# Performance work log

Hardware: AMD Instinct MI355X
Metric: run time of the kernel (lower is better)

## Reference

```python
import jax, jax.numpy as jnp
import numpy as np

DIM = 128
N_CENTERS = 30
CUT_LO, CUT_HI = 0.0, 10.0
N_CONV = 3
NODE_VOCAB = 100
EDGE_VOCAB = 500
N_NODES = 50000
N_EDGES = 800000
N_GRAPHS = 100
DIM_E = DIM + N_CENTERS  # 158


def setup_inputs() -> dict:
    key = jax.random.key(0)
    ks = jax.random.split(key, 20)
    def xav(k, shape):
        fan_in = shape[-2] if len(shape) >= 2 else shape[-1]
        return (jax.random.normal(k, shape, dtype=jnp.float32) / np.sqrt(fan_in)).astype(jnp.float32)
    inp = {
        'node_types': jax.random.randint(ks[0], (N_NODES,), 0, NODE_VOCAB),
        'edge_types': jax.random.randint(ks[1], (N_EDGES,), 0, EDGE_VOCAB),
        'src': jax.random.randint(ks[2], (N_EDGES,), 0, N_NODES),
        'dst': jax.random.randint(ks[3], (N_EDGES,), 0, N_NODES),
        'graph_ids': jnp.sort(jax.random.randint(ks[4], (N_NODES,), 0, N_GRAPHS)),
        'distances': jax.random.uniform(ks[5], (N_EDGES,), dtype=jnp.float32, minval=CUT_LO, maxval=CUT_HI),
        'n_graphs': N_GRAPHS,
        # embedding tables
        'node_emb': xav(ks[6], (NODE_VOCAB, DIM)),
        'edge_emb': xav(ks[7], (EDGE_VOCAB, DIM)),
        # stacked per-conv-layer weights (n_conv leading dim)
        'Wn1': xav(ks[8], (N_CONV, DIM, DIM)),  'bn1': jnp.zeros((N_CONV, DIM), jnp.float32),
        'Wn2': xav(ks[9], (N_CONV, DIM, DIM)),  'bn2': jnp.zeros((N_CONV, DIM), jnp.float32),
        'We1': xav(ks[10], (N_CONV, DIM_E, DIM)), 'be1': jnp.zeros((N_CONV, DIM), jnp.float32),
        'We2': xav(ks[11], (N_CONV, DIM, DIM)),  'be2': jnp.zeros((N_CONV, DIM), jnp.float32),
        'Wc':  xav(ks[12], (N_CONV, DIM, DIM)),  'bc': jnp.zeros((N_CONV, DIM), jnp.float32),
        # read layer
        'Wr1': xav(ks[13], (DIM, DIM)), 'br1': jnp.zeros((DIM,), jnp.float32),
        'Wr2': xav(ks[14], (DIM, 1)),   'br2': jnp.zeros((1,), jnp.float32),
    }
    return inp


def reference(node_types, edge_types, src, dst, graph_ids, distances, n_graphs,
              node_emb, edge_emb, Wn1, bn1, Wn2, bn2, We1, be1, We2, be2, Wc, bc,
              Wr1, br1, Wr2, br2):
    # embeddings
    h = node_emb[node_types]                      # [N, D]
    e_emb = edge_emb[edge_types]                  # [E, D]
    # RBF expansion of distances
    centers = jnp.linspace(CUT_LO, CUT_HI, N_CENTERS, dtype=jnp.float32)
    gap = centers[1] - centers[0]
    rbf = jnp.exp(-((distances[:, None] - centers[None, :]) ** 2) / gap)  # [E, n_centers]
    e = jnp.concatenate([e_emb, rbf], axis=1)     # [E, D + n_centers]

    n_nodes = h.shape[0]
    for i in range(N_CONV):
        node_path = jnp.maximum(h[src] @ Wn1[i] + bn1[i], 0.0) @ Wn2[i] + bn2[i]   # [E, D]
        edge_path = jnp.maximum(e @ We1[i] + be1[i], 0.0) @ We2[i] + be2[i]        # [E, D]
        m = jnp.tanh((node_path * edge_path) @ Wc[i] + bc[i])                       # [E, D]
        h = h + jax.ops.segment_sum(m, dst, num_segments=n_nodes)                   # scatter-add to dst

    # readout MLP + per-graph node sum
    hr = jnp.maximum(h @ Wr1 + br1, 0.0) @ Wr2 + br2                                # [N, 1]
    out = jax.ops.segment_sum(hr, graph_ids, num_segments=n_graphs)                 # [G, 1]
    return out.reshape(-1)
```

## Files before the change

kernel.cpp:

```cpp
#include <hip/hip_runtime.h>
#include <stdint.h>

#define NNODES 50000
#define NEDGES 800000
#define NGRAPH 100
#define NCHUNK (NEDGES / 16)
#define NWAVES 4096
#define NB0 196

typedef _Float16 f16;
typedef __attribute__((ext_vector_type(8))) _Float16 half8;
typedef __attribute__((ext_vector_type(4))) _Float16 half4;
typedef __attribute__((ext_vector_type(4))) float floatx4;

__device__ __forceinline__ void stage_WT(const float* __restrict__ W, f16* WT,
                                         int tid, int nthr) {
    for (int idx = tid; idx < 128 * 32; idx += nthr) {
        int k = idx >> 5, n4 = (idx & 31) * 4;
        floatx4 v = *(const floatx4*)(W + k * 128 + n4);
        WT[(n4 + 0) * 136 + k] = (f16)v[0];
        WT[(n4 + 1) * 136 + k] = (f16)v[1];
        WT[(n4 + 2) * 136 + k] = (f16)v[2];
        WT[(n4 + 3) * 136 + k] = (f16)v[3];
    }
}

__device__ __forceinline__ float fast_tanh(float x) {
    x = fminf(fmaxf(x, -15.0f), 15.0f);
    float e2 = __expf(2.0f * x);
    return (e2 - 1.0f) * __builtin_amdgcn_rcpf(e2 + 1.0f);
}

__device__ __forceinline__ int mtAddr(int c, int rgroup) {
    return c * 16 + ((((c >> 2) + rgroup) & 3) << 2);
}

__global__ void init_k(float* out, int osz, int* cnt) {
    int i = blockIdx.x * 256 + threadIdx.x;
    if (i < osz) out[i] = 0.0f;
    if (i < NNODES) cnt[i] = 0;
}

__global__ void hist_k(const int* __restrict__ dst, int* __restrict__ cnt) {
    int e = blockIdx.x * 256 + threadIdx.x;
    if (e < NEDGES) atomicAdd(&cnt[dst[e]], 1);
}

__global__ __launch_bounds__(1024) void scan1_k(const int* __restrict__ cnt,
                                                int* __restrict__ rowStart,
                                                int* __restrict__ blockSum) {
    __shared__ int buf[1024];
    int tid = threadIdx.x;
    int i = blockIdx.x * 1024 + tid;
    int v = (i < NNODES) ? cnt[i] : 0;
    buf[tid] = v;
    __syncthreads();
    for (int off = 1; off < 1024; off <<= 1) {
        int t = (tid >= off) ? buf[tid - off] : 0;
        __syncthreads();
        buf[tid] += t;
        __syncthreads();
    }
    if (i < NNODES) rowStart[i] = buf[tid] - v;
    if (tid == 1023) blockSum[blockIdx.x] = buf[1023];
}

__global__ void scan2_k(int* __restrict__ blockSum, int nb) {
    if (threadIdx.x == 0) {
        int run = 0;
        for (int b = 0; b < nb; ++b) { int s = blockSum[b]; blockSum[b] = run; run += s; }
    }
}

__global__ __launch_bounds__(1024) void scan3_k(int* __restrict__ rowStart,
                                                const int* __restrict__ blockSum,
                                                int* __restrict__ cnt) {
    int i = blockIdx.x * 1024 + threadIdx.x;
    if (i < NNODES) { rowStart[i] += blockSum[blockIdx.x]; cnt[i] = 0; }
    if (i == 0) rowStart[NNODES] = NEDGES;
}

__global__ void scatter_k(const int* __restrict__ src, const int* __restrict__ et,
                          const int* __restrict__ dst, const float* __restrict__ dist,
                          const int* __restrict__ rowStart, int* __restrict__ cnt,
                          uint4* __restrict__ packE) {
    int e = blockIdx.x * 256 + threadIdx.x;
    if (e >= NEDGES) return;
    int d = dst[e];
    int pos = rowStart[d] + atomicAdd(&cnt[d], 1);
    uint4 pk;
    pk.x = (unsigned)src[e];
    pk.y = (unsigned)et[e];
    pk.z = (unsigned)d;
    pk.w = __float_as_uint(dist[e]);
    packE[pos] = pk;
}

__global__ void gather_h(const int* __restrict__ nt, const float* __restrict__ emb,
                         float* __restrict__ h) {
    int i = blockIdx.x * 256 + threadIdx.x;
    int row = i >> 5, c4 = (i & 31) * 4;
    if (row < NNODES)
        *(floatx4*)(h + row * 128 + c4) = *(const floatx4*)(emb + nt[row] * 128 + c4);
}

__global__ __launch_bounds__(1024, 4) void mlp_combo(
        const float* __restrict__ Xh,
        const float* __restrict__ W1, const float* __restrict__ b1,
        const float* __restrict__ W2, const float* __restrict__ b2,
        f16* __restrict__ OutP,
        const float* __restrict__ Xe,
        const float* __restrict__ We1, const float* __restrict__ be1,
        f16* __restrict__ OutT) {
    __shared__ f16 W1T[128 * 136];
    __shared__ f16 W2T[128 * 136];
    __shared__ f16 xBuf[256 * 136];
    __shared__ float bias1[128];
    __shared__ float bias2[128];
    int tid = threadIdx.x;
    bool mode2 = blockIdx.x >= NB0;

    const float* X  = mode2 ? Xe : Xh;
    const float* Wa = mode2 ? We1 : W1;
    const float* ba = mode2 ? be1 : b1;
    f16* Out        = mode2 ? OutT : OutP;
    int  M          = mode2 ? 500 : NNODES;
    int  r0         = (mode2 ? (blockIdx.x - NB0) : blockIdx.x) * 256;

    stage_WT(Wa, W1T, tid, 1024);
    if (!mode2) stage_WT(W2, W2T, tid, 1024);
    if (tid < 128) { bias1[tid] = ba[tid]; bias2[tid] = mode2 ? 0.0f : b2[tid]; }

    for (int it = 0; it < 8; ++it) {
        int row = it * 32 + (tid >> 5);
        int c4 = (tid & 31) * 4;
        int gr = r0 + row;
        floatx4 x = {0.0f, 0.0f, 0.0f, 0.0f};
        if (gr < M) x = *(const floatx4*)(X + (size_t)gr * 128 + c4);
        half4 xh;
        xh[0] = (f16)x[0]; xh[1] = (f16)x[1]; xh[2] = (f16)x[2]; xh[3] = (f16)x[3];
        *(half4*)(xBuf + row * 136 + c4) = xh;
    }
    __syncthreads();

    int lane = tid & 63, wv = tid >> 6;
    int R = wv * 16;
    int n16 = lane & 15, q = lane >> 4;
    int gr = r0 + R + n16;

    half8 a[4];
    #pragma unroll
    for (int kk = 0; kk < 4; ++kk)
        a[kk] = *(const half8*)(xBuf + (R + n16) * 136 + kk * 32 + q * 8);

    #pragma unroll
    for (int f = 0; f < 8; ++f) {
        floatx4 acc = *(const floatx4*)(bias1 + f * 16 + q * 4);
        #pragma unroll
        for (int kk = 0; kk < 4; ++kk) {
            half8 aw = *(const half8*)(W1T + (f * 16 + n16) * 136 + kk * 32 + q * 8);
            acc = __builtin_amdgcn_mfma_f32_16x16x32_f16(aw, a[kk], acc, 0, 0, 0);
        }
        if (!mode2) {
            half4 y;
            #pragma unroll
            for (int i = 0; i < 4; ++i) y[i] = (f16)fmaxf(acc[i], 0.0f);
            *(half4*)(xBuf + (R + n16) * 136 + f * 16 + q * 4) = y;
        } else {
            half4 o;
            #pragma unroll
            for (int i = 0; i < 4; ++i) o[i] = (f16)acc[i];
            if (gr < M) *(half4*)(Out + (size_t)gr * 128 + f * 16 + q * 4) = o;
        }
    }

    if (!mode2) {
        #pragma unroll
        for (int kk = 0; kk < 4; ++kk)
            a[kk] = *(const half8*)(xBuf + (R + n16) * 136 + kk * 32 + q * 8);
        #pragma unroll
        for (int f = 0; f < 8; ++f) {
            floatx4 acc = *(const floatx4*)(bias2 + f * 16 + q * 4);
            #pragma unroll
            for (int kk = 0; kk < 4; ++kk) {
                half8 aw = *(const half8*)(W2T + (f * 16 + n16) * 136 + kk * 32 + q * 8);
                acc = __builtin_amdgcn_mfma_f32_16x16x32_f16(aw, a[kk], acc, 0, 0, 0);
            }
            half4 o;
            #pragma unroll
            for (int i = 0; i < 4; ++i) o[i] = (f16)acc[i];
            if (gr < M) *(half4*)(Out + (size_t)gr * 128 + f * 16 + q * 4) = o;
        }
    }
}

__global__ __launch_bounds__(1024, 4) void edge_kernel(
        const uint4* __restrict__ packE,
        const f16* __restrict__ P, const f16* __restrict__ T,
        const float* __restrict__ We1,
        const float* __restrict__ We2, const float* __restrict__ be2,
        const float* __restrict__ Wc,  const float* __restrict__ bc,
        float* __restrict__ h) {
    __shared__ f16 W2T[128 * 136];
    __shared__ f16 WcT[128 * 136];
    __shared__ f16 W1rT[128 * 40];
    __shared__ f16 Uall[16 * 2176];
    __shared__ float sbe2[128], sbc[128];
    __shared__ int dstW[16][16];

    int tid = threadIdx.x;
    stage_WT(We2, W2T, tid, 1024);
    stage_WT(Wc,  WcT, tid, 1024);
    for (int idx = tid; idx < 128 * 32; idx += 1024) {
        int n = idx >> 5, kr = idx & 31;
        W1rT[n * 40 + kr] = (kr < 30) ? (f16)We1[(128 + kr) * 128 + n] : (f16)0.0f;
    }
    if (tid < 128) { sbe2[tid] = be2[tid]; sbc[tid] = bc[tid]; }
    __syncthreads();

    int lane = tid & 63, wv = tid >> 6;
    f16* U = Uall + wv * 2176;
    int* dW = dstW[wv];
    int n16 = lane & 15, q = lane >> 4;
    const float invgap = 29.0f / 10.0f;
    int colA = lane, colB = lane + 64;
    int tsub = lane & 3, trow = lane >> 2;

    float sbcv[8];
    #pragma unroll
    for (int f = 0; f < 8; ++f) sbcv[f] = sbc[f * 16 + n16];

    int wgid = blockIdx.x * 16 + wv;
    int extra = wgid < 848 ? wgid : 848;
    int c0 = wgid * 12 + extra;
    int c1 = c0 + 12 + (wgid < 848 ? 1 : 0);

    float carry0 = 0.0f, carry1 = 0.0f;
    int prev = -1;

    uint4 pk = {0u, 0u, 0u, 0u};
    if (lane < 16) pk = packE[(size_t)c0 * 16 + lane];

    for (int ch = c0; ch < c1; ++ch) {
        bool hasNext = (ch + 1 < c1);
        int   ety  = __shfl((int)pk.y, trow);
        int   srcv = __shfl((int)pk.x, n16);
        float dcur = __shfl(__uint_as_float(pk.w), n16);
        if (lane < 16) dW[lane] = (int)pk.z;

        {
            const uint4* Tp = (const uint4*)(T + (size_t)ety * 128 + tsub * 32);
            uint4 tr0 = Tp[0], tr1 = Tp[1], tr2 = Tp[2], tr3 = Tp[3];
            uint4* ub = (uint4*)(U + trow * 136 + tsub * 32);
            ub[0] = tr0; ub[1] = tr1; ub[2] = tr2; ub[3] = tr3;
        }
        __builtin_amdgcn_sched_barrier(0);

        half8 pA0, pA1, pA2, pA3;
        {
            const f16* Pr = P + (size_t)srcv * 128 + q * 8;
            pA0 = *(const half8*)(Pr);
            pA1 = *(const half8*)(Pr + 32);
            pA2 = *(const half8*)(Pr + 64);
            pA3 = *(const half8*)(Pr + 96);
        }
        uint4 pkn = {0u, 0u, 0u, 0u};
        if (hasNext && lane < 16) pkn = packE[(size_t)(ch + 1) * 16 + lane];

        half8 ar;
        #pragma unroll
        for (int j = 0; j < 8; ++j) {
            int k = q * 8 + j;
            float c = (float)k * (10.0f / 29.0f);
            float df = dcur - c;
            ar[j] = (f16)((k < 30) ? __expf(-df * df * invgap) : 0.0f);
        }

        #pragma unroll
        for (int f = 0; f < 8; ++f) {
            f16* up = U + n16 * 136 + f * 16 + q * 4;
            half4 tv = *(const half4*)up;
            floatx4 c4 = {(float)tv[0], (float)tv[1], (float)tv[2], (float)tv[3]};
            half8 aw = *(const half8*)(W1rT + (f * 16 + n16) * 40 + q * 8);
            c4 = __builtin_amdgcn_mfma_f32_16x16x32_f16(aw, ar, c4, 0, 0, 0);
            half4 uv;
            #pragma unroll
            for (int i = 0; i < 4; ++i) uv[i] = (f16)fmaxf(c4[i], 0.0f);
            *(half4*)up = uv;
        }

        half8 a2[4];
        #pragma unroll
        for (int kk = 0; kk < 4; ++kk)
            a2[kk] = *(const half8*)(U + n16 * 136 + kk * 32 + q * 8);
        #pragma unroll
        for (int f = 0; f < 8; ++f) {
            floatx4 acc = *(const floatx4*)(sbe2 + f * 16 + q * 4);
            #pragma unroll
            for (int kk = 0; kk < 4; ++kk) {
                half8 aw = *(const half8*)(W2T + (f * 16 + n16) * 136 + kk * 32 + q * 8);
                acc = __builtin_amdgcn_mfma_f32_16x16x32_f16(aw, a2[kk], acc, 0, 0, 0);
            }
            half4 ev;
            #pragma unroll
            for (int i = 0; i < 4; ++i) ev[i] = (f16)acc[i];
            *(half4*)(U + n16 * 136 + f * 16 + q * 4) = ev;
        }

        {
            half8 e0 = *(const half8*)(U + n16 * 136 + 0 * 32 + q * 8);
            half8 e1 = *(const half8*)(U + n16 * 136 + 1 * 32 + q * 8);
            half8 e2 = *(const half8*)(U + n16 * 136 + 2 * 32 + q * 8);
            half8 e3 = *(const half8*)(U + n16 * 136 + 3 * 32 + q * 8);
            a2[0] = e0 * pA0; a2[1] = e1 * pA1; a2[2] = e2 * pA2; a2[3] = e3 * pA3;
        }
        #pragma unroll
        for (int f = 0; f < 8; ++f) {
            float bb = sbcv[f];
            floatx4 acc = {bb, bb, bb, bb};
            #pragma unroll
            for (int kk = 0; kk < 4; ++kk) {
                half8 b = *(const half8*)(WcT + (f * 16 + n16) * 136 + kk * 32 + q * 8);
                acc = __builtin_amdgcn_mfma_f32_16x16x32_f16(a2[kk], b, acc, 0, 0, 0);
            }
            int c = f * 16 + n16;
            half4 mv;
            #pragma unroll
            for (int i = 0; i < 4; ++i) mv[i] = (f16)fast_tanh(acc[i]);
            *(half4*)(U + mtAddr(c, q)) = mv;
        }

        {
            half4 va[4], vb[4];
            #pragma unroll
            for (int g2 = 0; g2 < 4; ++g2) {
                va[g2] = *(const half4*)(U + mtAddr(colA, g2));
                vb[g2] = *(const half4*)(U + mtAddr(colB, g2));
            }
            int dArr[16];
            *(int4*)(dArr)      = *(const int4*)(dW);
            *(int4*)(dArr + 4)  = *(const int4*)(dW + 4);
            *(int4*)(dArr + 8)  = *(const int4*)(dW + 8);
            *(int4*)(dArr + 12) = *(const int4*)(dW + 12);
            #pragma unroll
            for (int r = 0; r < 16; ++r) {
                int dd = dArr[r];
                float v0 = (float)va[r >> 2][r & 3];
                float v1 = (float)vb[r >> 2][r & 3];
                if (dd != prev) {
                    if (prev >= 0) {
                        unsafeAtomicAdd(&h[(size_t)prev * 128 + colA], carry0);
                        unsafeAtomicAdd(&h[(size_t)prev * 128 + colB], carry1);
                    }
                    prev = dd; carry0 = v0; carry1 = v1;
                } else { carry0 += v0; carry1 += v1; }
            }
        }
        pk = pkn;
        __builtin_amdgcn_sched_barrier(0);
    }
    if (prev >= 0) {
        unsafeAtomicAdd(&h[(size_t)prev * 128 + colA], carry0);
        unsafeAtomicAdd(&h[(size_t)prev * 128 + colB], carry1);
    }
}

__global__ __launch_bounds__(1024, 4) void readout_k(
        const float* __restrict__ X, int M,
        const float* __restrict__ W1, const float* __restrict__ b1,
        const float* __restrict__ Wr2, const float* __restrict__ br2,
        const int* __restrict__ gid, float* __restrict__ out) {
    __shared__ f16 W1T[128 * 136];
    __shared__ f16 xBuf[256 * 136];
    __shared__ float bias1[128];
    __shared__ float sWr2[128];
    int tid = threadIdx.x;

    stage_WT(W1, W1T, tid, 1024);
    if (tid < 128) { bias1[tid] = b1[tid]; sWr2[tid] = Wr2[tid]; }

    int r0 = blockIdx.x * 256;
    for (int it = 0; it < 8; ++it) {
        int row = it * 32 + (tid >> 5);
        int c4 = (tid & 31) * 4;
        int gr = r0 + row;
        floatx4 x = {0.0f, 0.0f, 0.0f, 0.0f};
        if (gr < M) x = *(const floatx4*)(X + (size_t)gr * 128 + c4);
        half4 xh;
        xh[0] = (f16)x[0]; xh[1] = (f16)x[1]; xh[2] = (f16)x[2]; xh[3] = (f16)x[3];
        *(half4*)(xBuf + row * 136 + c4) = xh;
    }
    __syncthreads();

    int lane = tid & 63, wv = tid >> 6;
    int R = wv * 16;
    int n16 = lane & 15, q = lane >> 4;

    half8 a[4];
    #pragma unroll
    for (int kk = 0; kk < 4; ++kk)
        a[kk] = *(const half8*)(xBuf + (R + n16) * 136 + kk * 32 + q * 8);

    floatx4 acc[8];
    #pragma unroll
    for (int f = 0; f < 8; ++f) {
        float bb = bias1[f * 16 + n16];
        acc[f] = (floatx4){bb, bb, bb, bb};
        #pragma unroll
        for (int kk = 0; kk < 4; ++kk) {
            half8 b = *(const half8*)(W1T + (f * 16 + n16) * 136 + kk * 32 + q * 8);
            acc[f] = __builtin_amdgcn_mfma_f32_16x16x32_f16(a[kk], b, acc[f], 0, 0, 0);
        }
    }

    float s[4];
    #pragma unroll
    for (int i = 0; i < 4; ++i) {
        float t = 0.0f;
        #pragma unroll
        for (int f = 0; f < 8; ++f)
            t += fmaxf(acc[f][i], 0.0f) * sWr2[f * 16 + n16];
        #pragma unroll
        for (int m = 1; m < 16; m <<= 1) t += __shfl_xor(t, m);
        s[i] = t;
    }

    if (n16 == 0) {
        float br2v = br2[0];
        float t = 0.0f; int g = -1;
        #pragma unroll
        for (int i = 0; i < 4; ++i) {
            int gr = r0 + R + q * 4 + i;
            if (gr < M) {
                int gi = gid[gr];
                float si = s[i] + br2v;
                if (gi == g) t += si;
                else { if (g >= 0) unsafeAtomicAdd(&out[g], t); g = gi; t = si; }
            }
        }
        if (g >= 0) unsafeAtomicAdd(&out[g], t);
    }
}

extern "C" void kernel_launch(void* const* d_in, const int* in_sizes, int n_in,
                              void* d_out, int out_size, void* d_ws, size_t ws_size,
                              hipStream_t stream) {
    (void)in_sizes; (void)n_in; (void)ws_size;
    const int*   node_types = (const int*)d_in[0];
    const int*   edge_types = (const int*)d_in[1];
    const int*   src        = (const int*)d_in[2];
    const int*   dst        = (const int*)d_in[3];
    const int*   graph_ids  = (const int*)d_in[4];
    const float* distances  = (const float*)d_in[5];
    const float* node_emb   = (const float*)d_in[7];
    const float* edge_emb   = (const float*)d_in[8];
    const float* Wn1 = (const float*)d_in[9];
    const float* bn1 = (const float*)d_in[10];
    const float* Wn2 = (const float*)d_in[11];
    const float* bn2 = (const float*)d_in[12];
    const float* We1 = (const float*)d_in[13];
    const float* be1 = (const float*)d_in[14];
    const float* We2 = (const float*)d_in[15];
    const float* be2 = (const float*)d_in[16];
    const float* Wc  = (const float*)d_in[17];
    const float* bc  = (const float*)d_in[18];
    const float* Wr1 = (const float*)d_in[19];
    const float* br1 = (const float*)d_in[20];
    const float* Wr2 = (const float*)d_in[21];
    const float* br2 = (const float*)d_in[22];

    char* w = (char*)d_ws;
    auto carve = [&](size_t bytes) { char* p = w; w += (bytes + 255) & ~(size_t)255; return p; };
    float* h        = (float*)carve((size_t)NNODES * 128 * 4);
    f16*   P        = (f16*)  carve((size_t)NNODES * 128 * 2);
    f16*   T        = (f16*)  carve((size_t)500 * 128 * 2);
    int*   rowStart = (int*)  carve((size_t)(NNODES + 1) * 4);
    int*   cnt      = (int*)  carve((size_t)NNODES * 4);
    int*   blockSum = (int*)  carve((size_t)64 * 4);
    uint4* packE    = (uint4*)carve((size_t)NEDGES * 16);

    float* out = (float*)d_out;
    const int NB1 = (NNODES + 1023) / 1024;

    init_k<<<(NNODES + 255) / 256, 256, 0, stream>>>(out, out_size, cnt);
    hist_k<<<NEDGES / 256, 256, 0, stream>>>(dst, cnt);
    scan1_k<<<NB1, 1024, 0, stream>>>(cnt, rowStart, blockSum);
    scan2_k<<<1, 64, 0, stream>>>(blockSum, NB1);
    scan3_k<<<NB1, 1024, 0, stream>>>(rowStart, blockSum, cnt);
    scatter_k<<<NEDGES / 256, 256, 0, stream>>>(src, edge_types, dst, distances,
                                                rowStart, cnt, packE);
    gather_h<<<(NNODES * 32 + 255) / 256, 256, 0, stream>>>(node_types, node_emb, h);

    for (int i = 0; i < 3; ++i) {
        mlp_combo<<<NB0 + 2, 1024, 0, stream>>>(
            h, Wn1 + (size_t)i * 128 * 128, bn1 + i * 128,
            Wn2 + (size_t)i * 128 * 128, bn2 + i * 128, P,
            edge_emb, We1 + (size_t)i * 158 * 128, be1 + i * 128, T);
        edge_kernel<<<256, 1024, 0, stream>>>(
            packE, P, T,
            We1 + (size_t)i * 158 * 128,
            We2 + (size_t)i * 128 * 128, be2 + i * 128,
            Wc + (size_t)i * 128 * 128, bc + i * 128, h);
    }

    readout_k<<<(NNODES + 255) / 256, 1024, 0, stream>>>(
        h, NNODES, Wr1, br1, Wr2, br2, graph_ids, out);
}
```

Before: 678.8 us.

## Fuse CSR preprocessing kernels into one cooperative kernel with grid syncs

Replaces seven small preprocessing launches (init, histogram, three-stage scan, scatter, embedding gather) with a single cooperative kernel that uses grid-wide syncs between phases. The serial single-thread block-sum scan becomes a wavefront shuffle scan, and the embedding gather now overlaps with the histogram phase. This is meant to remove launch gaps and tail idle time. The cost is five grid barriers and fewer threads per phase (256 blocks striding over the work), and cooperative launch requires all 256 blocks of 1024 threads to be resident at once.

```diff
diff --git a/kernel.cpp b/kernel.cpp
--- a/kernel.cpp
+++ b/kernel.cpp
@@ -1,5 +1,8 @@
 #include <hip/hip_runtime.h>
+#include <hip/hip_cooperative_groups.h>
 #include <stdint.h>
+
+namespace cg = cooperative_groups;
 
 #define NNODES 50000
 #define NEDGES 800000
@@ -7,6 +10,7 @@
 #define NCHUNK (NEDGES / 16)
 #define NWAVES 4096
 #define NB0 196
+#define NSCAN 49
 
 typedef _Float16 f16;
 typedef __attribute__((ext_vector_type(8))) _Float16 half8;
@@ -35,73 +39,77 @@
     return c * 16 + ((((c >> 2) + rgroup) & 3) << 2);
 }
 
-__global__ void init_k(float* out, int osz, int* cnt) {
-    int i = blockIdx.x * 256 + threadIdx.x;
-    if (i < osz) out[i] = 0.0f;
-    if (i < NNODES) cnt[i] = 0;
-}
-
-__global__ void hist_k(const int* __restrict__ dst, int* __restrict__ cnt) {
-    int e = blockIdx.x * 256 + threadIdx.x;
-    if (e < NEDGES) atomicAdd(&cnt[dst[e]], 1);
-}
-
-__global__ __launch_bounds__(1024) void scan1_k(const int* __restrict__ cnt,
-                                                int* __restrict__ rowStart,
-                                                int* __restrict__ blockSum) {
+__global__ __launch_bounds__(1024) void coop_prep(
+        const int* __restrict__ nt, const float* __restrict__ emb,
+        float* __restrict__ h,
+        const int* __restrict__ src, const int* __restrict__ et,
+        const int* __restrict__ dst, const float* __restrict__ dist,
+        int* __restrict__ cnt, int* __restrict__ rowStart,
+        int* __restrict__ blockSum, uint4* __restrict__ packE,
+        float* __restrict__ out, int osz) {
+    cg::grid_group grid = cg::this_grid();
     __shared__ int buf[1024];
     int tid = threadIdx.x;
-    int i = blockIdx.x * 1024 + tid;
-    int v = (i < NNODES) ? cnt[i] : 0;
-    buf[tid] = v;
-    __syncthreads();
-    for (int off = 1; off < 1024; off <<= 1) {
-        int t = (tid >= off) ? buf[tid - off] : 0;
+    int gtid = blockIdx.x * 1024 + tid;
+    const int GSZ = 256 * 1024;
+
+    for (int i = gtid; i < NNODES; i += GSZ) cnt[i] = 0;
+    if (gtid < osz) out[gtid] = 0.0f;
+    grid.sync();
+
+    for (int i = gtid; i < NNODES * 32; i += GSZ) {
+        int row = i >> 5, c4 = (i & 31) * 4;
+        *(floatx4*)(h + (size_t)row * 128 + c4) =
+            *(const floatx4*)(emb + (size_t)nt[row] * 128 + c4);
+    }
+    for (int e = gtid; e < NEDGES; e += GSZ) atomicAdd(&cnt[dst[e]], 1);
+    grid.sync();
+
+    if (blockIdx.x < NSCAN) {
+        int i = blockIdx.x * 1024 + tid;
+        int v = (i < NNODES) ? cnt[i] : 0;
+        buf[tid] = v;
         __syncthreads();
-        buf[tid] += t;
-        __syncthreads();
-    }
-    if (i < NNODES) rowStart[i] = buf[tid] - v;
-    if (tid == 1023) blockSum[blockIdx.x] = buf[1023];
-}
-
-__global__ void scan2_k(int* __restrict__ blockSum, int nb) {
-    if (threadIdx.x == 0) {
-        int run = 0;
-        for (int b = 0; b < nb; ++b) { int s = blockSum[b]; blockSum[b] = run; run += s; }
-    }
-}
-
-__global__ __launch_bounds__(1024) void scan3_k(int* __restrict__ rowStart,
-                                                const int* __restrict__ blockSum,
-                                                int* __restrict__ cnt) {
-    int i = blockIdx.x * 1024 + threadIdx.x;
-    if (i < NNODES) { rowStart[i] += blockSum[blockIdx.x]; cnt[i] = 0; }
-    if (i == 0) rowStart[NNODES] = NEDGES;
-}
-
-__global__ void scatter_k(const int* __restrict__ src, const int* __restrict__ et,
-                          const int* __restrict__ dst, const float* __restrict__ dist,
-                          const int* __restrict__ rowStart, int* __restrict__ cnt,
-                          uint4* __restrict__ packE) {
-    int e = blockIdx.x * 256 + threadIdx.x;
-    if (e >= NEDGES) return;
-    int d = dst[e];
-    int pos = rowStart[d] + atomicAdd(&cnt[d], 1);
-    uint4 pk;
-    pk.x = (unsigned)src[e];
-    pk.y = (unsigned)et[e];
-    pk.z = (unsigned)d;
-    pk.w = __float_as_uint(dist[e]);
-    packE[pos] = pk;
-}
-
-__global__ void gather_h(const int* __restrict__ nt, const float* __restrict__ emb,
-                         float* __restrict__ h) {
-    int i = blockIdx.x * 256 + threadIdx.x;
-    int row = i >> 5, c4 = (i & 31) * 4;
-    if (row < NNODES)
-        *(floatx4*)(h + row * 128 + c4) = *(const floatx4*)(emb + nt[row] * 128 + c4);
+        for (int off = 1; off < 1024; off <<= 1) {
+            int t = (tid >= off) ? buf[tid - off] : 0;
+            __syncthreads();
+            buf[tid] += t;
+            __syncthreads();
+        }
+        if (i < NNODES) rowStart[i] = buf[tid] - v;
+        if (tid == 1023) blockSum[blockIdx.x] = buf[1023];
+    }
+    grid.sync();
+
+    if (blockIdx.x == 0 && tid < 64) {
+        int v = (tid < NSCAN) ? blockSum[tid] : 0;
+        int inc = v;
+        #pragma unroll
+        for (int d = 1; d < 64; d <<= 1) {
+            int t = __shfl_up(inc, d);
+            if ((tid & 63) >= d) inc += t;
+        }
+        if (tid < NSCAN) blockSum[tid] = inc - v;
+    }
+    grid.sync();
+
+    for (int i = gtid; i < NNODES; i += GSZ) {
+        rowStart[i] += blockSum[i >> 10];
+        cnt[i] = 0;
+    }
+    if (gtid == 0) rowStart[NNODES] = NEDGES;
+    grid.sync();
+
+    for (int e = gtid; e < NEDGES; e += GSZ) {
+        int d = dst[e];
+        int pos = rowStart[d] + atomicAdd(&cnt[d], 1);
+        uint4 pk;
+        pk.x = (unsigned)src[e];
+        pk.y = (unsigned)et[e];
+        pk.z = (unsigned)d;
+        pk.w = __float_as_uint(dist[e]);
+        packE[pos] = pk;
+    }
 }
 
 __global__ __launch_bounds__(1024, 4) void mlp_combo(
@@ -480,16 +488,15 @@
     uint4* packE    = (uint4*)carve((size_t)NEDGES * 16);
 
     float* out = (float*)d_out;
-    const int NB1 = (NNODES + 1023) / 1024;
-
-    init_k<<<(NNODES + 255) / 256, 256, 0, stream>>>(out, out_size, cnt);
-    hist_k<<<NEDGES / 256, 256, 0, stream>>>(dst, cnt);
-    scan1_k<<<NB1, 1024, 0, stream>>>(cnt, rowStart, blockSum);
-    scan2_k<<<1, 64, 0, stream>>>(blockSum, NB1);
-    scan3_k<<<NB1, 1024, 0, stream>>>(rowStart, blockSum, cnt);
-    scatter_k<<<NEDGES / 256, 256, 0, stream>>>(src, edge_types, dst, distances,
-                                                rowStart, cnt, packE);
-    gather_h<<<(NNODES * 32 + 255) / 256, 256, 0, stream>>>(node_types, node_emb, h);
+    int osz = out_size;
+
+    void* cargs[] = {
+        (void*)&node_types, (void*)&node_emb, (void*)&h,
+        (void*)&src, (void*)&edge_types, (void*)&dst, (void*)&distances,
+        (void*)&cnt, (void*)&rowStart, (void*)&blockSum, (void*)&packE,
+        (void*)&out, (void*)&osz };
+    hipLaunchCooperativeKernel((void*)coop_prep, dim3(256), dim3(1024),
+                               cargs, 0, stream);
 
     for (int i = 0; i < 3; ++i) {
         mlp_combo<<<NB0 + 2, 1024, 0, stream>>>(
```

Measured after the change: 838.0 us. 1.23x slower.
